# Optimization experiments

Hardware: AMD Instinct MI355X
Metric: run time of the kernel (lower is better)

The kernel has to match this reference:

```python
import jax, jax.numpy as jnp
import numpy as np

N = 8192
D_IN = 512
D_OUT = 256
ALPHA = 0.2
NEG = -9e15


def setup_inputs() -> dict:
    key = jax.random.key(0)
    k1, k2, k3, k4 = jax.random.split(key, 4)
    node = jax.random.normal(k1, (N, D_IN), dtype=jnp.float32)
    adj = jax.random.randint(k2, (N, N), 0, 2, dtype=jnp.int32)
    # xavier_uniform with gain=1.414
    gain = 1.414
    lim_w = gain * np.sqrt(6.0 / (D_IN + D_OUT))
    weight = jax.random.uniform(k3, (D_IN, D_OUT), minval=-lim_w, maxval=lim_w, dtype=jnp.float32)
    lim_a = gain * np.sqrt(6.0 / (2 * D_OUT + 1))
    a = jax.random.uniform(k4, (2 * D_OUT, 1), minval=-lim_a, maxval=lim_a, dtype=jnp.float32)
    bias = jnp.zeros((D_OUT,), dtype=jnp.float32)
    return {"node": node, "adj": adj, "weight": weight, "a": a, "bias": bias}


def reference(node, adj, weight, a, bias):
    # v: [N, D_OUT]
    v = node @ weight
    # per-node attention scalars: Q, K are [N, 1]
    Q = v @ a[:D_OUT, :]
    K = v @ a[D_OUT:, :]
    e = jax.nn.leaky_relu(Q + K.T, negative_slope=ALPHA)  # [N, N]
    attention = jnp.where(adj > 0, e, NEG)
    attention = jax.nn.softmax(attention, axis=1)
    # dropout is identity in eval mode (self.training == False)
    out = attention @ v  # [N, D_OUT]
    out = jax.nn.leaky_relu(out, negative_slope=ALPHA)
    # F.normalize(p=2, dim=1): x / max(||x||_2, 1e-12)
    norm = jnp.linalg.norm(out, axis=1, keepdims=True)
    out = out / jnp.maximum(norm, 1e-12)
    return out + bias
```

## Files before the change

kernel.cpp:

```cpp
#include <hip/hip_runtime.h>
#include <hip/hip_bf16.h>

#define N_NODES 8192
#define DIN     512
#define DOUT    256
#define ALPHA   0.2f
#define LOG2E   1.4426950408889634f

typedef __bf16 bf16x8 __attribute__((ext_vector_type(8)));
typedef __bf16 bf16x4 __attribute__((ext_vector_type(4)));
typedef float  f32x4  __attribute__((ext_vector_type(4)));
typedef int    i32x4  __attribute__((ext_vector_type(4)));
typedef unsigned u32x4 __attribute__((ext_vector_type(4)));

__global__ __launch_bounds__(256) void k_repack_w(const float* __restrict__ w,
                                                  bf16x8* __restrict__ wB,
                                                  unsigned* __restrict__ kmaxkey) {
    if (blockIdx.x == 0 && threadIdx.x == 0) *kmaxkey = 0u;
    int u = blockIdx.x * 256 + threadIdx.x;
    int lane = u & 63, t = u >> 6;
    int nt = t & 15, kt = t >> 4;
    int k0 = kt * 32 + (lane >> 4) * 8;
    int col = nt * 16 + (lane & 15);
    bf16x8 r;
#pragma unroll
    for (int i = 0; i < 8; ++i) r[i] = (__bf16)w[(size_t)(k0 + i) * DOUT + col];
    wB[u] = r;
}

__global__ __launch_bounds__(256) void k_gemm1f(const float* __restrict__ node,
                                                const bf16x8* __restrict__ wB,
                                                const float* __restrict__ a,
                                                bf16x8* __restrict__ vBo,
                                                float* __restrict__ Q, float* __restrict__ K,
                                                unsigned* __restrict__ kmaxkey) {
    __shared__ __bf16 vsh[32][260];
    __shared__ float qksh[32][2];
    int lane = threadIdx.x & 63, w = threadIdx.x >> 6;
    int r15 = lane & 15, g = lane >> 4;
    int nh = w & 1, rh = w >> 1;
    int rowbase = blockIdx.x * 32;
    int myrow = rowbase + rh * 16 + r15;
    const float* np = node + (size_t)myrow * DIN + g * 8;

    f32x4 acc[8];
#pragma unroll
    for (int j = 0; j < 8; ++j) acc[j] = (f32x4){0.f, 0.f, 0.f, 0.f};

    f32x4 c0 = *(const f32x4*)np;
    f32x4 c1 = *(const f32x4*)(np + 4);
    f32x4 c2 = *(const f32x4*)(np + 32);
    f32x4 c3 = *(const f32x4*)(np + 36);
    const bf16x8* wp = wB + (size_t)(nh * 8) * 64 + lane;
    bf16x8 fr0 = wp[0], fr1 = wp[64], fr2 = wp[128], fr3 = wp[192];
    bf16x8 fr4 = wp[256], fr5 = wp[320], fr6 = wp[384], fr7 = wp[448];

    for (int kt = 0; kt < 16; ++kt) {
        f32x4 u0 = c0, u1 = c1;
        c0 = c2; c1 = c3;
        if (kt + 2 < 16) {
            c2 = *(const f32x4*)(np + (kt + 2) * 32);
            c3 = *(const f32x4*)(np + (kt + 2) * 32 + 4);
        }
        bf16x8 f0 = fr0, f1 = fr1, f2 = fr2, f3 = fr3;
        bf16x8 f4 = fr4, f5 = fr5, f6 = fr6, f7 = fr7;
        if (kt + 1 < 16) {
            const bf16x8* wn = wB + ((size_t)(kt + 1) * 16 + nh * 8) * 64 + lane;
            fr0 = wn[0]; fr1 = wn[64]; fr2 = wn[128]; fr3 = wn[192];
            fr4 = wn[256]; fr5 = wn[320]; fr6 = wn[384]; fr7 = wn[448];
        }
        bf16x8 af;
#pragma unroll
        for (int i = 0; i < 4; ++i) { af[i] = (__bf16)u0[i]; af[i + 4] = (__bf16)u1[i]; }
        acc[0] = __builtin_amdgcn_mfma_f32_16x16x32_bf16(af, f0, acc[0], 0, 0, 0);
        acc[1] = __builtin_amdgcn_mfma_f32_16x16x32_bf16(af, f1, acc[1], 0, 0, 0);
        acc[2] = __builtin_amdgcn_mfma_f32_16x16x32_bf16(af, f2, acc[2], 0, 0, 0);
        acc[3] = __builtin_amdgcn_mfma_f32_16x16x32_bf16(af, f3, acc[3], 0, 0, 0);
        acc[4] = __builtin_amdgcn_mfma_f32_16x16x32_bf16(af, f4, acc[4], 0, 0, 0);
        acc[5] = __builtin_amdgcn_mfma_f32_16x16x32_bf16(af, f5, acc[5], 0, 0, 0);
        acc[6] = __builtin_amdgcn_mfma_f32_16x16x32_bf16(af, f6, acc[6], 0, 0, 0);
        acc[7] = __builtin_amdgcn_mfma_f32_16x16x32_bf16(af, f7, acc[7], 0, 0, 0);
    }

    float qp0 = 0.f, qp1 = 0.f, qp2 = 0.f, qp3 = 0.f;
    float kp0 = 0.f, kp1 = 0.f, kp2 = 0.f, kp3 = 0.f;
#pragma unroll
    for (int j = 0; j < 8; ++j) {
        int col = (nh * 8 + j) * 16 + r15;
        float a1 = a[col], a2 = a[DOUT + col];
        qp0 += acc[j][0] * a1; qp1 += acc[j][1] * a1;
        qp2 += acc[j][2] * a1; qp3 += acc[j][3] * a1;
        kp0 += acc[j][0] * a2; kp1 += acc[j][1] * a2;
        kp2 += acc[j][2] * a2; kp3 += acc[j][3] * a2;
    }
#pragma unroll
    for (int m = 1; m < 16; m <<= 1) {
        qp0 += __shfl_xor(qp0, m); qp1 += __shfl_xor(qp1, m);
        qp2 += __shfl_xor(qp2, m); qp3 += __shfl_xor(qp3, m);
        kp0 += __shfl_xor(kp0, m); kp1 += __shfl_xor(kp1, m);
        kp2 += __shfl_xor(kp2, m); kp3 += __shfl_xor(kp3, m);
    }

#pragma unroll
    for (int j = 0; j < 8; ++j)
#pragma unroll
        for (int r = 0; r < 4; ++r)
            vsh[rh * 16 + g * 4 + r][(nh * 8 + j) * 16 + r15] = (__bf16)acc[j][r];
    if (nh == 0 && r15 == 0) {
        int rl = rh * 16 + g * 4;
        qksh[rl + 0][0] = qp0; qksh[rl + 1][0] = qp1; qksh[rl + 2][0] = qp2; qksh[rl + 3][0] = qp3;
        qksh[rl + 0][1] = kp0; qksh[rl + 1][1] = kp1; qksh[rl + 2][1] = kp2; qksh[rl + 3][1] = kp3;
    }
    __syncthreads();
    if (nh == 1 && r15 == 0) {
        int rl = rh * 16 + g * 4;
        int rw = rowbase + rl;
        float q0 = qp0 + qksh[rl + 0][0], q1 = qp1 + qksh[rl + 1][0];
        float q2 = qp2 + qksh[rl + 2][0], q3 = qp3 + qksh[rl + 3][0];
        float k0 = kp0 + qksh[rl + 0][1], k1 = kp1 + qksh[rl + 1][1];
        float k2 = kp2 + qksh[rl + 2][1], k3 = kp3 + qksh[rl + 3][1];
        Q[rw + 0] = q0; Q[rw + 1] = q1; Q[rw + 2] = q2; Q[rw + 3] = q3;
        K[rw + 0] = k0; K[rw + 1] = k1; K[rw + 2] = k2; K[rw + 3] = k3;
        float km = fmaxf(fmaxf(k0, k1), fmaxf(k2, k3));
        unsigned bits = __float_as_uint(km);
        unsigned key = (bits & 0x80000000u) ? ~bits : (bits | 0x80000000u);
        atomicMax(kmaxkey, key);
    }
#pragma unroll
    for (int uu = 0; uu < 4; ++uu) {
        int nt = w * 4 + uu;
        bf16x8 t;
#pragma unroll
        for (int i = 0; i < 8; ++i) t[i] = vsh[g * 8 + i][nt * 16 + r15];
        vBo[((size_t)blockIdx.x * 16 + nt) * 64 + lane] = t;
    }
}

template<int JS>
__global__ __launch_bounds__(256, 2) void k_attn(const int* __restrict__ adj,
                                                 const bf16x8* __restrict__ vBg,
                                                 const float* __restrict__ Q,
                                                 const float* __restrict__ K,
                                                 const unsigned* __restrict__ kmaxkey,
                                                 __bf16* __restrict__ accB,
                                                 float* __restrict__ Sp) {
    constexpr int JR   = N_NODES / JS;
    constexpr int BIT  = JR / 32;
    constexpr int NG   = BIT / 4;
    constexpr int MSTR = BIT + 4;
    __shared__ float    Ks[JR];
    __shared__ unsigned Ms[64][MSTR];
    __shared__ bf16x8   pT[2][4][64];

    int bid = blockIdx.x;
    int rb = bid / JS, p = bid % JS;
    int lane = threadIdx.x & 63, w = threadIdx.x >> 6;
    int r15 = lane & 15, g = lane >> 4;
    int rowbase = rb * 64;
    int prow = rowbase + w * 16 + r15;
    int j0 = p * JR;

    for (int s = threadIdx.x * 4; s < JR; s += 1024)
        *(f32x4*)&Ks[s] = *(const f32x4*)&K[j0 + s];

    const int hrow = w * 2 + (lane >> 5);
    const int* abase = adj + (size_t)(rowbase + hrow) * N_NODES + j0 + (lane & 31) * 4;

#define ISSUE8(L, GG) { _Pragma("unroll")                                        \
    for (int q = 0; q < 8; ++q)                                                  \
        L[q] = *(const i32x4*)(abase + (size_t)(q * 8) * N_NODES + (GG) * 128); }

#define PACKB(L, GG) { _Pragma("unroll") for (int q = 0; q < 8; ++q) {           \
    unsigned long long b0_ = __ballot(L[q][0] != 0);                             \
    unsigned long long b1_ = __ballot(L[q][1] != 0);                             \
    unsigned long long b2_ = __ballot(L[q][2] != 0);                             \
    unsigned long long b3_ = __ballot(L[q][3] != 0);                             \
    if ((lane & 31) == 0) {                                                      \
        int hi_ = lane >> 5;                                                     \
        u32x4 u_;                                                                \
        u_[0] = hi_ ? (unsigned)(b0_ >> 32) : (unsigned)b0_;                     \
        u_[1] = hi_ ? (unsigned)(b1_ >> 32) : (unsigned)b1_;                     \
        u_[2] = hi_ ? (unsigned)(b2_ >> 32) : (unsigned)b2_;                     \
        u_[3] = hi_ ? (unsigned)(b3_ >> 32) : (unsigned)b3_;                     \
        *(u32x4*)&Ms[q * 8 + hrow][(GG) * 4] = u_;                               \
    } } }

    i32x4 La[8];
    {
        i32x4 Lb[8];
        ISSUE8(La, 0)
        ISSUE8(Lb, 1)
        PACKB(La, 0)
        PACKB(Lb, 1)
    }
    ISSUE8(La, 2)

    float qi = Q[prow];
    unsigned kk = *kmaxkey;
    unsigned kb = (kk & 0x80000000u) ? (kk ^ 0x80000000u) : ~kk;
    float kmax = __uint_as_float(kb);
    float t0 = qi + kmax;
    float c2 = fmaxf(t0, ALPHA * t0) * LOG2E;
    float qiL = qi * LOG2E;
    float A1 = qiL - c2;
    float A2 = ALPHA * qiL - c2;

    const bf16x8* vbp = vBg + ((size_t)(p * BIT) * 16 + w * 4) * 64 + lane;

    f32x4 acc[4][4];
#pragma unroll
    for (int m = 0; m < 4; ++m)
#pragma unroll
        for (int n = 0; n < 4; ++n) acc[m][n] = (f32x4){0.f, 0.f, 0.f, 0.f};
    float sl = 0.f;

    asm volatile("s_waitcnt lgkmcnt(0)" ::: "memory");
    __builtin_amdgcn_s_barrier();
    asm volatile("" ::: "memory");

    u32x4 Uc = *(const u32x4*)&Ms[w * 16 + r15][0];
    bf16x8 vS0 = vbp[0],    vS1 = vbp[64],   vS2 = vbp[128],  vS3 = vbp[192];
    bf16x8 vT0 = vbp[1024], vT1 = vbp[1088], vT2 = vbp[1152], vT3 = vbp[1216];

#define BODYM(UU, S, V0, V1, V2, V3, BUF, itv)                                  \
    {                                                                           \
        bf16x8 b0 = V0, b1 = V1, b2 = V2, b3 = V3;                              \
        if ((itv) + 2 < BIT) {                                                  \
            V0 = vbp[((itv) + 2) * 1024];       V1 = vbp[((itv) + 2) * 1024 + 64];  \
            V2 = vbp[((itv) + 2) * 1024 + 128]; V3 = vbp[((itv) + 2) * 1024 + 192]; \
        }                                                                       \
        f32x4 q0 = *(const f32x4*)&Ks[(itv) * 32 + g * 8];                      \
        f32x4 q1 = *(const f32x4*)&Ks[(itv) * 32 + g * 8 + 4];                  \
        unsigned bsh = (S) * 8 + g * 2;                                         \
        unsigned m0 = UU[0] >> bsh, m1 = UU[1] >> bsh;                          \
        unsigned m2 = UU[2] >> bsh, m3 = UU[3] >> bsh;                          \
        bf16x8 af;                                                              \
        _Pragma("unroll")                                                       \
        for (int i = 0; i < 8; ++i) {                                           \
            float kj = (i < 4) ? q0[i] : q1[i - 4];                             \
            float f1 = __builtin_fmaf(kj, LOG2E, A1);                           \
            float f2 = __builtin_fmaf(kj, ALPHA * LOG2E, A2);                   \
            float pv = __builtin_amdgcn_exp2f(fmaxf(f1, f2));                   \
            unsigned mm_ = (i & 3) == 0 ? m0 : ((i & 3) == 1 ? m1 : ((i & 3) == 2 ? m2 : m3)); \
            pv = (mm_ & (1u << (i >> 2))) ? pv : 0.f;                           \
            sl += pv;                                                           \
            af[i] = (__bf16)pv;                                                 \
        }                                                                       \
        pT[BUF][w][lane] = af;                                                  \
        asm volatile("s_waitcnt lgkmcnt(0)" ::: "memory");                      \
        __builtin_amdgcn_s_barrier();                                           \
        asm volatile("" ::: "memory");                                         \
        bf16x8 pa0 = pT[BUF][0][lane], pa1 = pT[BUF][1][lane];                  \
        bf16x8 pa2 = pT[BUF][2][lane], pa3 = pT[BUF][3][lane];                  \
        acc[0][0] = __builtin_amdgcn_mfma_f32_16x16x32_bf16(pa0, b0, acc[0][0], 0, 0, 0); \
        acc[0][1] = __builtin_amdgcn_mfma_f32_16x16x32_bf16(pa0, b1, acc[0][1], 0, 0, 0); \
        acc[0][2] = __builtin_amdgcn_mfma_f32_16x16x32_bf16(pa0, b2, acc[0][2], 0, 0, 0); \
        acc[0][3] = __builtin_amdgcn_mfma_f32_16x16x32_bf16(pa0, b3, acc[0][3], 0, 0, 0); \
        acc[1][0] = __builtin_amdgcn_mfma_f32_16x16x32_bf16(pa1, b0, acc[1][0], 0, 0, 0); \
        acc[1][1] = __builtin_amdgcn_mfma_f32_16x16x32_bf16(pa1, b1, acc[1][1], 0, 0, 0); \
        acc[1][2] = __builtin_amdgcn_mfma_f32_16x16x32_bf16(pa1, b2, acc[1][2], 0, 0, 0); \
        acc[1][3] = __builtin_amdgcn_mfma_f32_16x16x32_bf16(pa1, b3, acc[1][3], 0, 0, 0); \
        acc[2][0] = __builtin_amdgcn_mfma_f32_16x16x32_bf16(pa2, b0, acc[2][0], 0, 0, 0); \
        acc[2][1] = __builtin_amdgcn_mfma_f32_16x16x32_bf16(pa2, b1, acc[2][1], 0, 0, 0); \
        acc[2][2] = __builtin_amdgcn_mfma_f32_16x16x32_bf16(pa2, b2, acc[2][2], 0, 0, 0); \
        acc[2][3] = __builtin_amdgcn_mfma_f32_16x16x32_bf16(pa2, b3, acc[2][3], 0, 0, 0); \
        acc[3][0] = __builtin_amdgcn_mfma_f32_16x16x32_bf16(pa3, b0, acc[3][0], 0, 0, 0); \
        acc[3][1] = __builtin_amdgcn_mfma_f32_16x16x32_bf16(pa3, b1, acc[3][1], 0, 0, 0); \
        acc[3][2] = __builtin_amdgcn_mfma_f32_16x16x32_bf16(pa3, b2, acc[3][2], 0, 0, 0); \
        acc[3][3] = __builtin_amdgcn_mfma_f32_16x16x32_bf16(pa3, b3, acc[3][3], 0, 0, 0); \
    }

    for (int G = 0; G < NG; ++G) {
        const int it4 = G * 4;
        u32x4 Un = Uc;
        if (G + 1 < NG) Un = *(const u32x4*)&Ms[w * 16 + r15][it4 + 4];
        BODYM(Uc, 0, vS0, vS1, vS2, vS3, 0, it4 + 0)
        BODYM(Uc, 1, vT0, vT1, vT2, vT3, 1, it4 + 1)
        if (G + 2 < NG) {
            PACKB(La, G + 2)
            if (G + 3 < NG) ISSUE8(La, G + 3)
        }
        BODYM(Uc, 2, vS0, vS1, vS2, vS3, 0, it4 + 2)
        BODYM(Uc, 3, vT0, vT1, vT2, vT3, 1, it4 + 3)
        Uc = Un;
    }
#undef BODYM
#undef ISSUE8
#undef PACKB

    sl += __shfl_xor(sl, 16);
    sl += __shfl_xor(sl, 32);
    if (g == 0) Sp[(size_t)p * N_NODES + prow] = sl;

    __bf16* apb = accB + ((size_t)p * N_NODES + rowbase) * DOUT;
#pragma unroll
    for (int m = 0; m < 4; ++m)
#pragma unroll
        for (int r = 0; r < 4; ++r) {
            bf16x4 t2;
#pragma unroll
            for (int n = 0; n < 4; ++n) t2[n] = (__bf16)acc[m][n][r];
            *(bf16x4*)&apb[(size_t)(m * 16 + g * 4 + r) * DOUT + w * 64 + r15 * 4] = t2;
        }
}

template<int JS>
__global__ __launch_bounds__(256) void k_final(const __bf16* __restrict__ accB,
                                               const float* __restrict__ Sp,
                                               const float* __restrict__ bias,
                                               float* __restrict__ out) {
    int lane = threadIdx.x & 63, wv = threadIdx.x >> 6;
    int row = blockIdx.x * 4 + wv;
    float s = 0.f;
    f32x4 av = (f32x4){0.f, 0.f, 0.f, 0.f};
#pragma unroll
    for (int pp = 0; pp < JS; ++pp) {
        bf16x4 t = *(const bf16x4*)&accB[((size_t)pp * N_NODES + row) * DOUT + lane * 4];
#pragma unroll
        for (int j = 0; j < 4; ++j) av[j] += (float)t[j];
        s += Sp[(size_t)pp * N_NODES + row];
    }
    float inv = 1.0f / fmaxf(s, 1e-30f);
    f32x4 o;
#pragma unroll
    for (int j = 0; j < 4; ++j) {
        float x = av[j] * inv;
        o[j] = fmaxf(x, ALPHA * x);
    }
    float sq = o[0] * o[0] + o[1] * o[1] + o[2] * o[2] + o[3] * o[3];
#pragma unroll
    for (int m = 1; m < 64; m <<= 1) sq += __shfl_xor(sq, m);
    float innrm = 1.0f / fmaxf(sqrtf(sq), 1e-12f);
#pragma unroll
    for (int j = 0; j < 4; ++j) {
        int col = (lane >> 4) * 64 + j * 16 + (lane & 15);
        out[(size_t)row * DOUT + col] = o[j] * innrm + bias[col];
    }
}

extern "C" void kernel_launch(void* const* d_in, const int* in_sizes, int n_in,
                              void* d_out, int out_size, void* d_ws, size_t ws_size,
                              hipStream_t stream) {
    const float* node   = (const float*)d_in[0];
    const int*   adj    = (const int*)d_in[1];
    const float* weight = (const float*)d_in[2];
    const float* a      = (const float*)d_in[3];
    const float* bias   = (const float*)d_in[4];
    float* out = (float*)d_out;

    const size_t fixed  = 4522240;
    const size_t per_js = 32768 + (size_t)N_NODES * DOUT * 2;
    int js = (ws_size >= fixed + 8 * per_js) ? 8 : 4;

    char* ws = (char*)d_ws;
    bf16x8*   wB      = (bf16x8*)(ws);
    bf16x8*   vB      = (bf16x8*)(ws + 262144);
    float*    Q       = (float*)(ws + 4456448);
    float*    K       = (float*)(ws + 4489216);
    unsigned* kmaxkey = (unsigned*)(ws + 4521984);
    float*    Sp      = (float*)(ws + fixed);
    __bf16*   accB    = (__bf16*)(ws + fixed + (size_t)js * 32768);

    k_repack_w<<<dim3(64),  dim3(256), 0, stream>>>(weight, wB, kmaxkey);
    k_gemm1f  <<<dim3(256), dim3(256), 0, stream>>>(node, wB, a, vB, Q, K, kmaxkey);
    if (js == 8) {
        k_attn<8><<<dim3(128 * 8), dim3(256), 0, stream>>>(adj, vB, Q, K, kmaxkey, accB, Sp);
        k_final<8><<<dim3(2048), dim3(256), 0, stream>>>(accB, Sp, bias, out);
    } else {
        k_attn<4><<<dim3(128 * 4), dim3(256), 0, stream>>>(adj, vB, Q, K, kmaxkey, accB, Sp);
        k_final<4><<<dim3(2048), dim3(256), 0, stream>>>(accB, Sp, bias, out);
    }
}
```

Baseline: 113.0 us.

## Compute all 64 rows' probabilities per wave to drop per-step LDS exchange barriers

Previously each wave computed the probability tile for its own 16 rows, then shared it through LDS with a barrier at every k-step, so every wave could multiply all four row tiles against its column slice of V. Now each wave recomputes the exp/mask values for all four 16-row tiles itself and feeds them straight into the MFMAs, which removes the per-step LDS round trip and barrier. The adjacency bitmask buffer becomes double-buffered with a single barrier per group of four steps. This costs 4x redundant exp2 and VALU work per wave and more registers (four sets of row constants and partial sums), which may raise pressure under the two-blocks-per-CU launch bound.

```diff
diff --git a/kernel.cpp b/kernel.cpp
--- a/kernel.cpp
+++ b/kernel.cpp
@@ -12,6 +12,8 @@
 typedef float  f32x4  __attribute__((ext_vector_type(4)));
 typedef int    i32x4  __attribute__((ext_vector_type(4)));
 typedef unsigned u32x4 __attribute__((ext_vector_type(4)));
+
+#define MFMA16 __builtin_amdgcn_mfma_f32_16x16x32_bf16
 
 __global__ __launch_bounds__(256) void k_repack_w(const float* __restrict__ w,
                                                   bf16x8* __restrict__ wB,
@@ -72,14 +74,14 @@
         bf16x8 af;
 #pragma unroll
         for (int i = 0; i < 4; ++i) { af[i] = (__bf16)u0[i]; af[i + 4] = (__bf16)u1[i]; }
-        acc[0] = __builtin_amdgcn_mfma_f32_16x16x32_bf16(af, f0, acc[0], 0, 0, 0);
-        acc[1] = __builtin_amdgcn_mfma_f32_16x16x32_bf16(af, f1, acc[1], 0, 0, 0);
-        acc[2] = __builtin_amdgcn_mfma_f32_16x16x32_bf16(af, f2, acc[2], 0, 0, 0);
-        acc[3] = __builtin_amdgcn_mfma_f32_16x16x32_bf16(af, f3, acc[3], 0, 0, 0);
-        acc[4] = __builtin_amdgcn_mfma_f32_16x16x32_bf16(af, f4, acc[4], 0, 0, 0);
-        acc[5] = __builtin_amdgcn_mfma_f32_16x16x32_bf16(af, f5, acc[5], 0, 0, 0);
-        acc[6] = __builtin_amdgcn_mfma_f32_16x16x32_bf16(af, f6, acc[6], 0, 0, 0);
-        acc[7] = __builtin_amdgcn_mfma_f32_16x16x32_bf16(af, f7, acc[7], 0, 0, 0);
+        acc[0] = MFMA16(af, f0, acc[0], 0, 0, 0);
+        acc[1] = MFMA16(af, f1, acc[1], 0, 0, 0);
+        acc[2] = MFMA16(af, f2, acc[2], 0, 0, 0);
+        acc[3] = MFMA16(af, f3, acc[3], 0, 0, 0);
+        acc[4] = MFMA16(af, f4, acc[4], 0, 0, 0);
+        acc[5] = MFMA16(af, f5, acc[5], 0, 0, 0);
+        acc[6] = MFMA16(af, f6, acc[6], 0, 0, 0);
+        acc[7] = MFMA16(af, f7, acc[7], 0, 0, 0);
     }
 
     float qp0 = 0.f, qp1 = 0.f, qp2 = 0.f, qp3 = 0.f;
@@ -137,31 +139,25 @@
 }
 
 template<int JS>
-__global__ __launch_bounds__(256, 2) void k_attn(const int* __restrict__ adj,
-                                                 const bf16x8* __restrict__ vBg,
-                                                 const float* __restrict__ Q,
-                                                 const float* __restrict__ K,
-                                                 const unsigned* __restrict__ kmaxkey,
-                                                 __bf16* __restrict__ accB,
-                                                 float* __restrict__ Sp) {
-    constexpr int JR   = N_NODES / JS;
-    constexpr int BIT  = JR / 32;
-    constexpr int NG   = BIT / 4;
-    constexpr int MSTR = BIT + 4;
+__global__ __launch_bounds__(256, 2) void k_attn6(const int* __restrict__ adj,
+                                                  const bf16x8* __restrict__ vBg,
+                                                  const float* __restrict__ Q,
+                                                  const float* __restrict__ K,
+                                                  const unsigned* __restrict__ kmaxkey,
+                                                  __bf16* __restrict__ accB,
+                                                  float* __restrict__ Sp) {
+    constexpr int JR  = N_NODES / JS;
+    constexpr int BIT = JR / 32;
+    constexpr int NG  = BIT / 4;
     __shared__ float    Ks[JR];
-    __shared__ unsigned Ms[64][MSTR];
-    __shared__ bf16x8   pT[2][4][64];
-
-    int bid = blockIdx.x;
-    int rb = bid / JS, p = bid % JS;
-    int lane = threadIdx.x & 63, w = threadIdx.x >> 6;
-    int r15 = lane & 15, g = lane >> 4;
-    int rowbase = rb * 64;
-    int prow = rowbase + w * 16 + r15;
-    int j0 = p * JR;
-
-    for (int s = threadIdx.x * 4; s < JR; s += 1024)
-        *(f32x4*)&Ks[s] = *(const f32x4*)&K[j0 + s];
+    __shared__ unsigned Ms2[2][64][12];
+
+    const int bid = blockIdx.x;
+    const int rb = bid / JS, p = bid % JS;
+    const int lane = threadIdx.x & 63, w = threadIdx.x >> 6;
+    const int r15 = lane & 15, g = lane >> 4;
+    const int rowbase = rb * 64;
+    const int j0 = p * JR;
 
     const int hrow = w * 2 + (lane >> 5);
     const int* abase = adj + (size_t)(rowbase + hrow) * N_NODES + j0 + (lane & 31) * 4;
@@ -170,7 +166,7 @@
     for (int q = 0; q < 8; ++q)                                                  \
         L[q] = *(const i32x4*)(abase + (size_t)(q * 8) * N_NODES + (GG) * 128); }
 
-#define PACKB(L, GG) { _Pragma("unroll") for (int q = 0; q < 8; ++q) {           \
+#define PACKB(L, SLOT) { _Pragma("unroll") for (int q = 0; q < 8; ++q) {         \
     unsigned long long b0_ = __ballot(L[q][0] != 0);                             \
     unsigned long long b1_ = __ballot(L[q][1] != 0);                             \
     unsigned long long b2_ = __ballot(L[q][2] != 0);                             \
@@ -182,115 +178,110 @@
         u_[1] = hi_ ? (unsigned)(b1_ >> 32) : (unsigned)b1_;                     \
         u_[2] = hi_ ? (unsigned)(b2_ >> 32) : (unsigned)b2_;                     \
         u_[3] = hi_ ? (unsigned)(b3_ >> 32) : (unsigned)b3_;                     \
-        *(u32x4*)&Ms[q * 8 + hrow][(GG) * 4] = u_;                               \
+        *(u32x4*)&Ms2[SLOT][q * 8 + hrow][0] = u_;                               \
     } } }
 
     i32x4 La[8];
-    {
-        i32x4 Lb[8];
-        ISSUE8(La, 0)
-        ISSUE8(Lb, 1)
-        PACKB(La, 0)
-        PACKB(Lb, 1)
-    }
-    ISSUE8(La, 2)
-
-    float qi = Q[prow];
+    ISSUE8(La, 0)
+
+    for (int s = threadIdx.x * 4; s < JR; s += 1024)
+        *(f32x4*)&Ks[s] = *(const f32x4*)&K[j0 + s];
+
     unsigned kk = *kmaxkey;
     unsigned kb = (kk & 0x80000000u) ? (kk ^ 0x80000000u) : ~kk;
     float kmax = __uint_as_float(kb);
-    float t0 = qi + kmax;
-    float c2 = fmaxf(t0, ALPHA * t0) * LOG2E;
-    float qiL = qi * LOG2E;
-    float A1 = qiL - c2;
-    float A2 = ALPHA * qiL - c2;
+    float A1[4], A2[4];
+#pragma unroll
+    for (int m = 0; m < 4; ++m) {
+        float q = Q[rowbase + m * 16 + r15];
+        float t0 = q + kmax;
+        float c2 = fmaxf(t0, ALPHA * t0) * LOG2E;
+        A1[m] = q * LOG2E - c2;
+        A2[m] = ALPHA * q * LOG2E - c2;
+    }
+
+    PACKB(La, 0)
+    ISSUE8(La, 1)
+
+    f32x4 acc[4][4];
+#pragma unroll
+    for (int m = 0; m < 4; ++m)
+#pragma unroll
+        for (int n = 0; n < 4; ++n) acc[m][n] = (f32x4){0.f, 0.f, 0.f, 0.f};
+    float sl[4] = {0.f, 0.f, 0.f, 0.f};
 
     const bf16x8* vbp = vBg + ((size_t)(p * BIT) * 16 + w * 4) * 64 + lane;
-
-    f32x4 acc[4][4];
-#pragma unroll
-    for (int m = 0; m < 4; ++m)
-#pragma unroll
-        for (int n = 0; n < 4; ++n) acc[m][n] = (f32x4){0.f, 0.f, 0.f, 0.f};
-    float sl = 0.f;
+    bf16x8 vS0 = vbp[0],    vS1 = vbp[64],   vS2 = vbp[128],  vS3 = vbp[192];
+    bf16x8 vT0 = vbp[1024], vT1 = vbp[1088], vT2 = vbp[1152], vT3 = vbp[1216];
 
     asm volatile("s_waitcnt lgkmcnt(0)" ::: "memory");
     __builtin_amdgcn_s_barrier();
     asm volatile("" ::: "memory");
 
-    u32x4 Uc = *(const u32x4*)&Ms[w * 16 + r15][0];
-    bf16x8 vS0 = vbp[0],    vS1 = vbp[64],   vS2 = vbp[128],  vS3 = vbp[192];
-    bf16x8 vT0 = vbp[1024], vT1 = vbp[1088], vT2 = vbp[1152], vT3 = vbp[1216];
-
-#define BODYM(UU, S, V0, V1, V2, V3, BUF, itv)                                  \
+#define STEP(S, V0, V1, V2, V3)                                                 \
     {                                                                           \
+        const int itv = it4 + (S);                                              \
         bf16x8 b0 = V0, b1 = V1, b2 = V2, b3 = V3;                              \
-        if ((itv) + 2 < BIT) {                                                  \
-            V0 = vbp[((itv) + 2) * 1024];       V1 = vbp[((itv) + 2) * 1024 + 64];  \
-            V2 = vbp[((itv) + 2) * 1024 + 128]; V3 = vbp[((itv) + 2) * 1024 + 192]; \
+        if (itv + 2 < BIT) {                                                    \
+            V0 = vbp[(itv + 2) * 1024];       V1 = vbp[(itv + 2) * 1024 + 64];  \
+            V2 = vbp[(itv + 2) * 1024 + 128]; V3 = vbp[(itv + 2) * 1024 + 192]; \
         }                                                                       \
-        f32x4 q0 = *(const f32x4*)&Ks[(itv) * 32 + g * 8];                      \
-        f32x4 q1 = *(const f32x4*)&Ks[(itv) * 32 + g * 8 + 4];                  \
-        unsigned bsh = (S) * 8 + g * 2;                                         \
-        unsigned m0 = UU[0] >> bsh, m1 = UU[1] >> bsh;                          \
-        unsigned m2 = UU[2] >> bsh, m3 = UU[3] >> bsh;                          \
-        bf16x8 af;                                                              \
+        f32x4 q0 = *(const f32x4*)&Ks[itv * 32 + g * 8];                        \
+        f32x4 q1 = *(const f32x4*)&Ks[itv * 32 + g * 8 + 4];                    \
+        const unsigned bsh = (S) * 8 + g * 2;                                   \
         _Pragma("unroll")                                                       \
-        for (int i = 0; i < 8; ++i) {                                           \
-            float kj = (i < 4) ? q0[i] : q1[i - 4];                             \
-            float f1 = __builtin_fmaf(kj, LOG2E, A1);                           \
-            float f2 = __builtin_fmaf(kj, ALPHA * LOG2E, A2);                   \
-            float pv = __builtin_amdgcn_exp2f(fmaxf(f1, f2));                   \
-            unsigned mm_ = (i & 3) == 0 ? m0 : ((i & 3) == 1 ? m1 : ((i & 3) == 2 ? m2 : m3)); \
-            pv = (mm_ & (1u << (i >> 2))) ? pv : 0.f;                           \
-            sl += pv;                                                           \
-            af[i] = (__bf16)pv;                                                 \
+        for (int m = 0; m < 4; ++m) {                                           \
+            unsigned m0 = Um[m][0] >> bsh, m1 = Um[m][1] >> bsh;                \
+            unsigned m2 = Um[m][2] >> bsh, m3 = Um[m][3] >> bsh;                \
+            bf16x8 pa;                                                          \
+            _Pragma("unroll")                                                   \
+            for (int i = 0; i < 8; ++i) {                                       \
+                float kj = (i < 4) ? q0[i] : q1[i - 4];                         \
+                float f1 = __builtin_fmaf(kj, LOG2E, A1[m]);                    \
+                float f2 = __builtin_fmaf(kj, ALPHA * LOG2E, A2[m]);            \
+                float pv = __builtin_amdgcn_exp2f(fmaxf(f1, f2));               \
+                unsigned mm_ = (i & 3) == 0 ? m0 : ((i & 3) == 1 ? m1 : ((i & 3) == 2 ? m2 : m3)); \
+                pv = (mm_ & (1u << (i >> 2))) ? pv : 0.f;                       \
+                sl[m] += pv;                                                    \
+                pa[i] = (__bf16)pv;                                             \
+            }                                                                   \
+            acc[m][0] = MFMA16(pa, b0, acc[m][0], 0, 0, 0);                     \
+            acc[m][1] = MFMA16(pa, b1, acc[m][1], 0, 0, 0);                     \
+            acc[m][2] = MFMA16(pa, b2, acc[m][2], 0, 0, 0);                     \
+            acc[m][3] = MFMA16(pa, b3, acc[m][3], 0, 0, 0);                     \
         }                                                                       \
-        pT[BUF][w][lane] = af;                                                  \
-        asm volatile("s_waitcnt lgkmcnt(0)" ::: "memory");                      \
-        __builtin_amdgcn_s_barrier();                                           \
-        asm volatile("" ::: "memory");                                         \
-        bf16x8 pa0 = pT[BUF][0][lane], pa1 = pT[BUF][1][lane];                  \
-        bf16x8 pa2 = pT[BUF][2][lane], pa3 = pT[BUF][3][lane];                  \
-        acc[0][0] = __builtin_amdgcn_mfma_f32_16x16x32_bf16(pa0, b0, acc[0][0], 0, 0, 0); \
-        acc[0][1] = __builtin_amdgcn_mfma_f32_16x16x32_bf16(pa0, b1, acc[0][1], 0, 0, 0); \
-        acc[0][2] = __builtin_amdgcn_mfma_f32_16x16x32_bf16(pa0, b2, acc[0][2], 0, 0, 0); \
-        acc[0][3] = __builtin_amdgcn_mfma_f32_16x16x32_bf16(pa0, b3, acc[0][3], 0, 0, 0); \
-        acc[1][0] = __builtin_amdgcn_mfma_f32_16x16x32_bf16(pa1, b0, acc[1][0], 0, 0, 0); \
-        acc[1][1] = __builtin_amdgcn_mfma_f32_16x16x32_bf16(pa1, b1, acc[1][1], 0, 0, 0); \
-        acc[1][2] = __builtin_amdgcn_mfma_f32_16x16x32_bf16(pa1, b2, acc[1][2], 0, 0, 0); \
-        acc[1][3] = __builtin_amdgcn_mfma_f32_16x16x32_bf16(pa1, b3, acc[1][3], 0, 0, 0); \
-        acc[2][0] = __builtin_amdgcn_mfma_f32_16x16x32_bf16(pa2, b0, acc[2][0], 0, 0, 0); \
-        acc[2][1] = __builtin_amdgcn_mfma_f32_16x16x32_bf16(pa2, b1, acc[2][1], 0, 0, 0); \
-        acc[2][2] = __builtin_amdgcn_mfma_f32_16x16x32_bf16(pa2, b2, acc[2][2], 0, 0, 0); \
-        acc[2][3] = __builtin_amdgcn_mfma_f32_16x16x32_bf16(pa2, b3, acc[2][3], 0, 0, 0); \
-        acc[3][0] = __builtin_amdgcn_mfma_f32_16x16x32_bf16(pa3, b0, acc[3][0], 0, 0, 0); \
-        acc[3][1] = __builtin_amdgcn_mfma_f32_16x16x32_bf16(pa3, b1, acc[3][1], 0, 0, 0); \
-        acc[3][2] = __builtin_amdgcn_mfma_f32_16x16x32_bf16(pa3, b2, acc[3][2], 0, 0, 0); \
-        acc[3][3] = __builtin_amdgcn_mfma_f32_16x16x32_bf16(pa3, b3, acc[3][3], 0, 0, 0); \
     }
 
     for (int G = 0; G < NG; ++G) {
         const int it4 = G * 4;
-        u32x4 Un = Uc;
-        if (G + 1 < NG) Un = *(const u32x4*)&Ms[w * 16 + r15][it4 + 4];
-        BODYM(Uc, 0, vS0, vS1, vS2, vS3, 0, it4 + 0)
-        BODYM(Uc, 1, vT0, vT1, vT2, vT3, 1, it4 + 1)
-        if (G + 2 < NG) {
-            PACKB(La, G + 2)
-            if (G + 3 < NG) ISSUE8(La, G + 3)
-        }
-        BODYM(Uc, 2, vS0, vS1, vS2, vS3, 0, it4 + 2)
-        BODYM(Uc, 3, vT0, vT1, vT2, vT3, 1, it4 + 3)
-        Uc = Un;
-    }
-#undef BODYM
+        u32x4 Um[4];
+#pragma unroll
+        for (int m = 0; m < 4; ++m)
+            Um[m] = *(const u32x4*)&Ms2[G & 1][m * 16 + r15][0];
+        if (G + 1 < NG) PACKB(La, (G + 1) & 1)
+        STEP(0, vS0, vS1, vS2, vS3)
+        STEP(1, vT0, vT1, vT2, vT3)
+        if (G + 2 < NG) ISSUE8(La, G + 2)
+        STEP(2, vS0, vS1, vS2, vS3)
+        STEP(3, vT0, vT1, vT2, vT3)
+        asm volatile("s_waitcnt lgkmcnt(0)" ::: "memory");
+        __builtin_amdgcn_s_barrier();
+        asm volatile("" ::: "memory");
+    }
+#undef STEP
 #undef ISSUE8
 #undef PACKB
 
-    sl += __shfl_xor(sl, 16);
-    sl += __shfl_xor(sl, 32);
-    if (g == 0) Sp[(size_t)p * N_NODES + prow] = sl;
+#pragma unroll
+    for (int m = 0; m < 4; ++m) {
+        sl[m] += __shfl_xor(sl[m], 16);
+        sl[m] += __shfl_xor(sl[m], 32);
+    }
+    if (w == 0 && lane < 16) {
+#pragma unroll
+        for (int m = 0; m < 4; ++m)
+            Sp[(size_t)p * N_NODES + rowbase + m * 16 + r15] = sl[m];
+    }
 
     __bf16* apb = accB + ((size_t)p * N_NODES + rowbase) * DOUT;
 #pragma unroll
@@ -364,10 +355,10 @@
     k_repack_w<<<dim3(64),  dim3(256), 0, stream>>>(weight, wB, kmaxkey);
     k_gemm1f  <<<dim3(256), dim3(256), 0, stream>>>(node, wB, a, vB, Q, K, kmaxkey);
     if (js == 8) {
-        k_attn<8><<<dim3(128 * 8), dim3(256), 0, stream>>>(adj, vB, Q, K, kmaxkey, accB, Sp);
+        k_attn6<8><<<dim3(128 * 8), dim3(256), 0, stream>>>(adj, vB, Q, K, kmaxkey, accB, Sp);
         k_final<8><<<dim3(2048), dim3(256), 0, stream>>>(accB, Sp, bias, out);
     } else {
-        k_attn<4><<<dim3(128 * 4), dim3(256), 0, stream>>>(adj, vB, Q, K, kmaxkey, accB, Sp);
+        k_attn6<4><<<dim3(128 * 4), dim3(256), 0, stream>>>(adj, vB, Q, K, kmaxkey, accB, Sp);
         k_final<4><<<dim3(2048), dim3(256), 0, stream>>>(accB, Sp, bias, out);
     }
 }
```

After: 441.3 us. +290.7%, slower.
